# Performance work log

Measured on AMD Instinct MI355X. Metric: run time of the kernel, lower is better.

The kernel has to match this reference:

```python
import jax, jax.numpy as jnp
import numpy as np

S, N, E, D, HG, OG, L, B, HR = 8, 100000, 1600000, 64, 64, 64, 3, 128, 128
BN_EPS = 1e-5


def _glorot(k, shape):
    fan = shape[-2] + shape[-1]
    return jax.random.normal(k, shape, jnp.float32) * np.sqrt(2.0 / fan)


def setup_inputs() -> dict:
    key = jax.random.key(0)
    ks = jax.random.split(key, 16)
    xs = jax.random.normal(ks[0], (S, N, D), jnp.float32)
    edge_index = jax.random.randint(ks[1], (S, 2, E), 0, N, dtype=jnp.int32)
    batch = jnp.sort(jax.random.randint(ks[2], (N,), 0, B, dtype=jnp.int32))
    return {
        "xs": xs,
        "edge_index": edge_index,
        "batch": batch,
        # per-timestep, per-layer GIN MLP params (input_gnn == hidden_gnn == 64)
        "W1": _glorot(ks[3], (S, L, D, HG)),
        "b1": jnp.zeros((S, L, HG), jnp.float32),
        "gamma": jnp.ones((S, L, HG), jnp.float32),
        "beta": jnp.zeros((S, L, HG), jnp.float32),
        "W2": _glorot(ks[4], (S, L, HG, HG)),
        "b2": jnp.zeros((S, L, HG), jnp.float32),
        "Wg": _glorot(ks[5], (HG, OG)),
        "bg": jnp.zeros((OG,), jnp.float32),
        "Wih": _glorot(ks[6], (HR, OG)),
        "Whh": _glorot(ks[7], (HR, HR)),
        "bih": jnp.zeros((HR,), jnp.float32),
        "bhh": jnp.zeros((HR,), jnp.float32),
        "Wr": _glorot(ks[8], (1, HR)),
        "br": jnp.zeros((1,), jnp.float32),
        "batch_size": B,
    }


def _gnn_forward(xs, edge_index, batch, W1, b1, gamma, beta, W2, b2, Wg, bg,
                 Wih, Whh, bih, bhh, Wr, br, batch_size):
    n = xs.shape[1]
    pooled = []
    for t in range(S):  # small fixed seq_len; each timestep has distinct params
        x = xs[t]
        src, dst = edge_index[t, 0], edge_index[t, 1]
        for l in range(L):
            # GIN (eps=0): h_i = MLP(x_i + sum_{j->i} x_j)
            agg = jax.ops.segment_sum(x[src], dst, num_segments=n)
            h = x + agg
            h = h @ W1[t, l] + b1[t, l]
            # BatchNorm1d (training-mode stats over nodes, biased var)
            mu = jnp.mean(h, axis=0)
            var = jnp.var(h, axis=0)
            h = (h - mu) * jax.lax.rsqrt(var + BN_EPS) * gamma[t, l] + beta[t, l]
            h = jnp.tanh(h)
            h = jnp.tanh(h @ W2[t, l] + b2[t, l])
            x = h
        g = jax.ops.segment_sum(x, batch, num_segments=batch_size)  # global_add_pool
        pooled.append(g @ Wg + bg)
    h_seq = jnp.stack(pooled, axis=0)  # [S, B, OG]

    def rnn_step(hprev, xt):
        hnew = jnp.tanh(xt @ Wih.T + bih + hprev @ Whh.T + bhh)
        return hnew, None

    h0 = jnp.zeros((batch_size, HR), h_seq.dtype)
    h_last, _ = jax.lax.scan(rnn_step, h0, h_seq)
    return jax.nn.sigmoid(h_last @ Wr.T + br)  # [B, 1]


def reference(xs, edge_index, batch, W1, b1, gamma, beta, W2, b2, Wg, bg,
              Wih, Whh, bih, bhh, Wr, br, batch_size):
    return _gnn_forward(xs, edge_index, batch, W1, b1, gamma, beta, W2, b2,
                        Wg, bg, Wih, Whh, bih, bhh, Wr, br, batch_size)
```

## Files before the change

kernel.cpp:

```cpp
#include <hip/hip_runtime.h>
#include <math.h>

#define SQ 8
#define NN 100000
#define EE 1600000
#define LL 3
#define BB 128
#define HRR 128
#define ROWS 16
#define TILE 64
#define NTILE ((NN + TILE - 1) / TILE)
#define NBLK ((NN + 255) / 256)

__device__ __forceinline__ float fast_tanh(float x) {
    x = fminf(fmaxf(x, -15.f), 15.f);
    float e = __expf(2.f * x);
    return (e - 1.f) * __builtin_amdgcn_rcpf(e + 1.f);
}


__global__ void k_hist(const int* __restrict__ dst, int* __restrict__ deg) {
    int e = blockIdx.x * blockDim.x + threadIdx.x;
    if (e < EE) atomicAdd(&deg[dst[e]], 1);
}

__global__ void k_scan1(const int* __restrict__ deg, int* __restrict__ excl,
                        int* __restrict__ bsums) {
    __shared__ int buf[256];
    int tid = threadIdx.x;
    int i = blockIdx.x * 256 + tid;
    int v = (i < NN) ? deg[i] : 0;
    buf[tid] = v;
    __syncthreads();
    for (int off = 1; off < 256; off <<= 1) {
        int t = (tid >= off) ? buf[tid - off] : 0;
        __syncthreads();
        buf[tid] += t;
        __syncthreads();
    }
    if (i < NN) excl[i] = buf[tid] - v;
    if (tid == 255) bsums[blockIdx.x] = buf[255];
}

__global__ void k_scan2(const int* __restrict__ bsums, int* __restrict__ boff) {
    __shared__ int buf[512];
    int tid = threadIdx.x;
    int v = (tid < NBLK) ? bsums[tid] : 0;
    buf[tid] = v;
    __syncthreads();
    for (int off = 1; off < 512; off <<= 1) {
        int t = (tid >= off) ? buf[tid - off] : 0;
        __syncthreads();
        buf[tid] += t;
        __syncthreads();
    }
    if (tid < NBLK) boff[tid] = buf[tid] - v;
}

__global__ void k_scan3(int* __restrict__ row_start, const int* __restrict__ boff,
                        int* __restrict__ cursor) {
    int tid = threadIdx.x;
    int i = blockIdx.x * 256 + tid;
    if (i < NN) {
        int r = row_start[i] + boff[blockIdx.x];
        row_start[i] = r;
        cursor[i] = r;
    }
    if (blockIdx.x == 0 && tid == 0) row_start[NN] = EE;
}

__global__ void k_fill(const int* __restrict__ src, const int* __restrict__ dst,
                       int* __restrict__ cursor, int* __restrict__ csr) {
    int e = blockIdx.x * blockDim.x + threadIdx.x;
    if (e < EE) {
        int d = dst[e];
        int p = atomicAdd(&cursor[d], 1);
        csr[p] = src[e];
    }
}


__global__ __launch_bounds__(256, 6) void k_agg_mlp1(
    const float* __restrict__ xin, const int* __restrict__ row_start,
    const int* __restrict__ csr, const float* __restrict__ W1,
    const float* __restrict__ b1, float* __restrict__ h_out,
    float* __restrict__ stats) {
    __shared__ float sW[4096];
    __shared__ float sSum[4][64];
    __shared__ float sSq[4][64];
    int tid = threadIdx.x;
    for (int k = tid; k < 4096; k += 256) sW[k] = W1[k];
    __syncthreads();
    int wave = tid >> 6, lane = tid & 63;
    float bias = b1[lane];
    int base = blockIdx.x * TILE + wave * ROWS;
    float aS = 0.f, aQ = 0.f;
    for (int r = 0; r < ROWS; r++) {
        int i = base + r;
        if (i >= NN) break;
        float s = xin[(size_t)i * 64 + lane];
        int e0 = row_start[i], e1 = row_start[i + 1];
        int eb = e0;
        while (eb < e1) {
            int m = e1 - eb; if (m > 64) m = 64;
            int id = (lane < m) ? csr[eb + lane] : 0;
            int k = 0;
            for (; k + 8 <= m; k += 8) {
                const size_t o = lane;
                float v0 = xin[(size_t)__shfl(id, k + 0, 64) * 64 + o];
                float v1 = xin[(size_t)__shfl(id, k + 1, 64) * 64 + o];
                float v2 = xin[(size_t)__shfl(id, k + 2, 64) * 64 + o];
                float v3 = xin[(size_t)__shfl(id, k + 3, 64) * 64 + o];
                float v4 = xin[(size_t)__shfl(id, k + 4, 64) * 64 + o];
                float v5 = xin[(size_t)__shfl(id, k + 5, 64) * 64 + o];
                float v6 = xin[(size_t)__shfl(id, k + 6, 64) * 64 + o];
                float v7 = xin[(size_t)__shfl(id, k + 7, 64) * 64 + o];
                s += ((v0 + v1) + (v2 + v3)) + ((v4 + v5) + (v6 + v7));
            }
            for (; k + 2 <= m; k += 2) {
                float v0 = xin[(size_t)__shfl(id, k + 0, 64) * 64 + lane];
                float v1 = xin[(size_t)__shfl(id, k + 1, 64) * 64 + lane];
                s += v0 + v1;
            }
            for (; k < m; k++) s += xin[(size_t)__shfl(id, k, 64) * 64 + lane];
            eb += m;
        }
        float h0 = bias, h1 = 0.f, h2 = 0.f, h3 = 0.f;
#pragma unroll
        for (int c = 0; c < 64; c += 4) {
            h0 = fmaf(__shfl(s, c + 0, 64), sW[(c + 0) * 64 + lane], h0);
            h1 = fmaf(__shfl(s, c + 1, 64), sW[(c + 1) * 64 + lane], h1);
            h2 = fmaf(__shfl(s, c + 2, 64), sW[(c + 2) * 64 + lane], h2);
            h3 = fmaf(__shfl(s, c + 3, 64), sW[(c + 3) * 64 + lane], h3);
        }
        float h = (h0 + h1) + (h2 + h3);
        h_out[(size_t)i * 64 + lane] = h;
        aS += h;
        aQ += h * h;
    }
    sSum[wave][lane] = aS;
    sSq[wave][lane] = aQ;
    __syncthreads();
    if (wave == 0) {
        float s4 = sSum[0][lane] + sSum[1][lane] + sSum[2][lane] + sSum[3][lane];
        float q4 = sSq[0][lane] + sSq[1][lane] + sSq[2][lane] + sSq[3][lane];
        atomicAdd(&stats[lane], s4);
        atomicAdd(&stats[64 + lane], q4);
    }
}


__global__ __launch_bounds__(256, 6) void k_bn_mlp2(
    const float* __restrict__ h_in, const float* __restrict__ W2,
    const float* __restrict__ b2, const float* __restrict__ gamma,
    const float* __restrict__ beta, const float* __restrict__ stats,
    float* __restrict__ x_out, float* __restrict__ g_pool,
    const int* __restrict__ batch) {
    __shared__ float sW[4096];
    int tid = threadIdx.x;
    for (int k = tid; k < 4096; k += 256) sW[k] = W2[k];
    __syncthreads();
    int wave = tid >> 6, lane = tid & 63;
    float bias = b2[lane];
    float mu = stats[lane] * (1.0f / NN);
    float var = stats[64 + lane] * (1.0f / NN) - mu * mu;
    float scale = rsqrtf(var + 1e-5f) * gamma[lane];
    float shift = beta[lane] - mu * scale;
    int base = blockIdx.x * TILE + wave * ROWS;
    float pacc = 0.f;
    int pbid = -1;
    for (int r = 0; r < ROWS; r++) {
        int i = base + r;
        if (i >= NN) break;
        float v = h_in[(size_t)i * 64 + lane];
        float s = fast_tanh(fmaf(v, scale, shift));
        float h0 = bias, h1 = 0.f, h2 = 0.f, h3 = 0.f;
#pragma unroll
        for (int c = 0; c < 64; c += 4) {
            h0 = fmaf(__shfl(s, c + 0, 64), sW[(c + 0) * 64 + lane], h0);
            h1 = fmaf(__shfl(s, c + 1, 64), sW[(c + 1) * 64 + lane], h1);
            h2 = fmaf(__shfl(s, c + 2, 64), sW[(c + 2) * 64 + lane], h2);
            h3 = fmaf(__shfl(s, c + 3, 64), sW[(c + 3) * 64 + lane], h3);
        }
        float o = fast_tanh((h0 + h1) + (h2 + h3));
        if (x_out) {
            x_out[(size_t)i * 64 + lane] = o;
        } else {
            int bid = batch[i];
            if (bid != pbid) {
                if (pbid >= 0) atomicAdd(&g_pool[pbid * 64 + lane], pacc);
                pacc = 0.f;
                pbid = bid;
            }
            pacc += o;
        }
    }
    if (g_pool && pbid >= 0) atomicAdd(&g_pool[pbid * 64 + lane], pacc);
}


__global__ void k_pool_proj(const float* __restrict__ g_all, const float* __restrict__ Wg,
                            const float* __restrict__ bg, float* __restrict__ seq) {
    int idx = blockIdx.x * 256 + threadIdx.x;
    int o = idx & 63, row = idx >> 6;
    float acc = bg[o];
    const float* g = g_all + (size_t)row * 64;
#pragma unroll 8
    for (int c = 0; c < 64; c++) acc = fmaf(g[c], Wg[c * 64 + o], acc);
    seq[idx] = acc;
}

__global__ void k_transpose(const float* __restrict__ in, float* __restrict__ out,
                            int rows, int cols) {
    int idx = blockIdx.x * blockDim.x + threadIdx.x;
    if (idx < rows * cols) {
        int r = idx / cols, c = idx % cols;
        out[c * rows + r] = in[idx];
    }
}

__global__ __launch_bounds__(128) void k_rnn_all(
    const float* __restrict__ seq, const float* __restrict__ WihT,
    const float* __restrict__ WhhT, const float* __restrict__ bih,
    const float* __restrict__ bhh, const float* __restrict__ Wr,
    const float* __restrict__ br, float* __restrict__ out) {
    int b = blockIdx.x, j = threadIdx.x;
    __shared__ float sh[128];
    __shared__ float sx[64];
    __shared__ float sp[128];
    sh[j] = 0.f;
    float bsum = bih[j] + bhh[j];
    __syncthreads();
    for (int t = 0; t < SQ; t++) {
        if (j < 64) sx[j] = seq[((size_t)t * BB + b) * 64 + j];
        __syncthreads();
        float acc = bsum;
#pragma unroll 16
        for (int c = 0; c < 64; c++) acc = fmaf(sx[c], WihT[c * 128 + j], acc);
#pragma unroll 16
        for (int k = 0; k < 128; k++) acc = fmaf(sh[k], WhhT[k * 128 + j], acc);
        acc = tanhf(acc);
        __syncthreads();
        sh[j] = acc;
        __syncthreads();
    }
    sp[j] = sh[j] * Wr[j];
    __syncthreads();
    if (j == 0) {
        float a = br[0];
        for (int k = 0; k < 128; k++) a += sp[k];
        out[b] = 1.f / (1.f + expf(-a));
    }
}


extern "C" void kernel_launch(void* const* d_in, const int* in_sizes, int n_in,
                              void* d_out, int out_size, void* d_ws, size_t ws_size,
                              hipStream_t stream) {
    const float* xs    = (const float*)d_in[0];
    const int*   edge  = (const int*)d_in[1];
    const int*   batch = (const int*)d_in[2];
    const float* W1    = (const float*)d_in[3];
    const float* b1    = (const float*)d_in[4];
    const float* gamma = (const float*)d_in[5];
    const float* beta  = (const float*)d_in[6];
    const float* W2    = (const float*)d_in[7];
    const float* b2    = (const float*)d_in[8];
    const float* Wg    = (const float*)d_in[9];
    const float* bg    = (const float*)d_in[10];
    const float* Wih   = (const float*)d_in[11];
    const float* Whh   = (const float*)d_in[12];
    const float* bih   = (const float*)d_in[13];
    const float* bhh   = (const float*)d_in[14];
    const float* Wr    = (const float*)d_in[15];
    const float* br    = (const float*)d_in[16];

    char* p = (char*)d_ws;
    auto alloc = [&](size_t bytes) -> char* {
        char* r = p;
        p += (bytes + 255) & ~(size_t)255;
        return r;
    };
    float* x_cur     = (float*)alloc((size_t)NN * 64 * 4);
    float* h_tmp     = (float*)alloc((size_t)NN * 64 * 4);
    float* g_all     = (float*)alloc((size_t)SQ * BB * 64 * 4);
    float* seq       = (float*)alloc((size_t)SQ * BB * 64 * 4);
    float* WihT      = (float*)alloc((size_t)64 * HRR * 4);
    float* WhhT      = (float*)alloc((size_t)HRR * HRR * 4);
    float* stats     = (float*)alloc((size_t)SQ * LL * 128 * 4);
    int*   row_start = (int*)alloc((size_t)(NN + 1) * 4);
    int*   cursor    = (int*)alloc((size_t)NN * 4);
    int*   deg       = (int*)alloc((size_t)NN * 4);
    int*   csr       = (int*)alloc((size_t)EE * 4);
    int*   bsums     = (int*)alloc(512 * 4);
    int*   boff      = (int*)alloc(512 * 4);

    hipMemsetAsync(stats, 0, (size_t)SQ * LL * 128 * 4, stream);
    hipMemsetAsync(g_all, 0, (size_t)SQ * BB * 64 * 4, stream);
    k_transpose<<<(128 * 64 + 255) / 256, 256, 0, stream>>>(Wih, WihT, 128, 64);
    k_transpose<<<(128 * 128 + 255) / 256, 256, 0, stream>>>(Whh, WhhT, 128, 128);

    int ghist = EE / 256;
    for (int t = 0; t < SQ; t++) {
        const int* src = edge + (size_t)t * 2 * EE;
        const int* dst = src + EE;
        hipMemsetAsync(deg, 0, (size_t)NN * 4, stream);
        k_hist<<<ghist, 256, 0, stream>>>(dst, deg);
        k_scan1<<<NBLK, 256, 0, stream>>>(deg, row_start, bsums);
        k_scan2<<<1, 512, 0, stream>>>(bsums, boff);
        k_scan3<<<NBLK, 256, 0, stream>>>(row_start, boff, cursor);
        k_fill<<<ghist, 256, 0, stream>>>(src, dst, cursor, csr);
        for (int l = 0; l < LL; l++) {
            int pl = t * LL + l;
            const float* xin = (l == 0) ? xs + (size_t)t * NN * 64 : x_cur;
            k_agg_mlp1<<<NTILE, 256, 0, stream>>>(xin, row_start, csr,
                                                  W1 + (size_t)pl * 4096, b1 + (size_t)pl * 64,
                                                  h_tmp, stats + (size_t)pl * 128);
            k_bn_mlp2<<<NTILE, 256, 0, stream>>>(h_tmp, W2 + (size_t)pl * 4096,
                                                 b2 + (size_t)pl * 64, gamma + (size_t)pl * 64,
                                                 beta + (size_t)pl * 64, stats + (size_t)pl * 128,
                                                 (l < 2) ? x_cur : nullptr,
                                                 (l == 2) ? (g_all + (size_t)t * BB * 64) : nullptr,
                                                 batch);
        }
    }
    k_pool_proj<<<SQ * BB * 64 / 256, 256, 0, stream>>>(g_all, Wg, bg, seq);
    k_rnn_all<<<BB, 128, 0, stream>>>(seq, WihT, WhhT, bih, bhh, Wr, br, (float*)d_out);
}
```

Before: 7.727 ms.

## Process four nodes per wave with float4 gathers in aggregation+MLP1 kernel

Rewrites the aggregation/MLP1 kernel so each wave handles four nodes at once, with 16 lanes per node each loading a float4 (16 bytes) of the feature row instead of one float per lane. Neighbor ids are fetched 16 at a time per node, and the loop runs until every node in the wave is done. The 64x64 matvec becomes a per-lane float4 output computation, and the BN statistics are reduced with xor shuffles before the atomics. This aims to cut per-edge instruction and latency overhead in the gather, at the cost of divergence when nodes in a wave have different degrees, and wasted masked loads on padded slots.

```diff
diff --git a/kernel.cpp b/kernel.cpp
--- a/kernel.cpp
+++ b/kernel.cpp
@@ -7,7 +7,6 @@
 #define LL 3
 #define BB 128
 #define HRR 128
-#define ROWS 16
 #define TILE 64
 #define NTILE ((NN + TILE - 1) / TILE)
 #define NBLK ((NN + 255) / 256)
@@ -86,66 +85,98 @@
     const float* __restrict__ b1, float* __restrict__ h_out,
     float* __restrict__ stats) {
     __shared__ float sW[4096];
-    __shared__ float sSum[4][64];
-    __shared__ float sSq[4][64];
+    __shared__ float4 sS[4][16];
+    __shared__ float4 sQ[4][16];
     int tid = threadIdx.x;
     for (int k = tid; k < 4096; k += 256) sW[k] = W1[k];
     __syncthreads();
     int wave = tid >> 6, lane = tid & 63;
-    float bias = b1[lane];
-    int base = blockIdx.x * TILE + wave * ROWS;
-    float aS = 0.f, aQ = 0.f;
-    for (int r = 0; r < ROWS; r++) {
-        int i = base + r;
-        if (i >= NN) break;
-        float s = xin[(size_t)i * 64 + lane];
-        int e0 = row_start[i], e1 = row_start[i + 1];
-        int eb = e0;
-        while (eb < e1) {
-            int m = e1 - eb; if (m > 64) m = 64;
-            int id = (lane < m) ? csr[eb + lane] : 0;
-            int k = 0;
-            for (; k + 8 <= m; k += 8) {
-                const size_t o = lane;
-                float v0 = xin[(size_t)__shfl(id, k + 0, 64) * 64 + o];
-                float v1 = xin[(size_t)__shfl(id, k + 1, 64) * 64 + o];
-                float v2 = xin[(size_t)__shfl(id, k + 2, 64) * 64 + o];
-                float v3 = xin[(size_t)__shfl(id, k + 3, 64) * 64 + o];
-                float v4 = xin[(size_t)__shfl(id, k + 4, 64) * 64 + o];
-                float v5 = xin[(size_t)__shfl(id, k + 5, 64) * 64 + o];
-                float v6 = xin[(size_t)__shfl(id, k + 6, 64) * 64 + o];
-                float v7 = xin[(size_t)__shfl(id, k + 7, 64) * 64 + o];
-                s += ((v0 + v1) + (v2 + v3)) + ((v4 + v5) + (v6 + v7));
+    int sub = lane & 15;
+    int gbase = lane & 48;
+    float4 b4 = *(const float4*)&b1[sub * 4];
+    float4 aS = {0.f, 0.f, 0.f, 0.f}, aQ = {0.f, 0.f, 0.f, 0.f};
+    int nbase = blockIdx.x * TILE + wave * 16;
+    for (int r = 0; r < 4; r++) {
+        int i = nbase + r * 4 + (gbase >> 4);
+        bool valid = (i < NN);
+        int e0 = 0, e1 = 0;
+        float4 s0 = {0.f, 0.f, 0.f, 0.f}, s1 = {0.f, 0.f, 0.f, 0.f};
+        if (valid) {
+            e0 = row_start[i];
+            e1 = row_start[i + 1];
+            s0 = *(const float4*)&xin[(size_t)i * 64 + sub * 4];
+        }
+        for (int eb = e0; __any(eb < e1); eb += 16) {
+            int e = eb + sub;
+            int id = (e < e1) ? csr[e] : 0;
+#pragma unroll
+            for (int k = 0; k < 16; k += 2) {
+                int nb0 = __shfl(id, gbase + k, 64);
+                int nb1 = __shfl(id, gbase + k + 1, 64);
+                bool v0 = (eb + k) < e1;
+                bool v1 = (eb + k + 1) < e1;
+                float4 t0 = *(const float4*)&xin[(size_t)(v0 ? nb0 : 0) * 64 + sub * 4];
+                float4 t1 = *(const float4*)&xin[(size_t)(v1 ? nb1 : 0) * 64 + sub * 4];
+                if (v0) { s0.x += t0.x; s0.y += t0.y; s0.z += t0.z; s0.w += t0.w; }
+                if (v1) { s1.x += t1.x; s1.y += t1.y; s1.z += t1.z; s1.w += t1.w; }
             }
-            for (; k + 2 <= m; k += 2) {
-                float v0 = xin[(size_t)__shfl(id, k + 0, 64) * 64 + lane];
-                float v1 = xin[(size_t)__shfl(id, k + 1, 64) * 64 + lane];
-                s += v0 + v1;
-            }
-            for (; k < m; k++) s += xin[(size_t)__shfl(id, k, 64) * 64 + lane];
-            eb += m;
-        }
-        float h0 = bias, h1 = 0.f, h2 = 0.f, h3 = 0.f;
+        }
+        float4 s;
+        s.x = s0.x + s1.x; s.y = s0.y + s1.y; s.z = s0.z + s1.z; s.w = s0.w + s1.w;
+        float4 h0 = b4, h1 = {0.f, 0.f, 0.f, 0.f};
 #pragma unroll
         for (int c = 0; c < 64; c += 4) {
-            h0 = fmaf(__shfl(s, c + 0, 64), sW[(c + 0) * 64 + lane], h0);
-            h1 = fmaf(__shfl(s, c + 1, 64), sW[(c + 1) * 64 + lane], h1);
-            h2 = fmaf(__shfl(s, c + 2, 64), sW[(c + 2) * 64 + lane], h2);
-            h3 = fmaf(__shfl(s, c + 3, 64), sW[(c + 3) * 64 + lane], h3);
-        }
-        float h = (h0 + h1) + (h2 + h3);
-        h_out[(size_t)i * 64 + lane] = h;
-        aS += h;
-        aQ += h * h;
-    }
-    sSum[wave][lane] = aS;
-    sSq[wave][lane] = aQ;
-    __syncthreads();
-    if (wave == 0) {
-        float s4 = sSum[0][lane] + sSum[1][lane] + sSum[2][lane] + sSum[3][lane];
-        float q4 = sSq[0][lane] + sSq[1][lane] + sSq[2][lane] + sSq[3][lane];
-        atomicAdd(&stats[lane], s4);
-        atomicAdd(&stats[64 + lane], q4);
+            int srcl = gbase + (c >> 2);
+            float scx = __shfl(s.x, srcl, 64);
+            float scy = __shfl(s.y, srcl, 64);
+            float scz = __shfl(s.z, srcl, 64);
+            float scw = __shfl(s.w, srcl, 64);
+            float4 w0 = *(const float4*)&sW[(c + 0) * 64 + sub * 4];
+            float4 w1 = *(const float4*)&sW[(c + 1) * 64 + sub * 4];
+            float4 w2 = *(const float4*)&sW[(c + 2) * 64 + sub * 4];
+            float4 w3 = *(const float4*)&sW[(c + 3) * 64 + sub * 4];
+            h0.x = fmaf(scx, w0.x, h0.x); h0.y = fmaf(scx, w0.y, h0.y);
+            h0.z = fmaf(scx, w0.z, h0.z); h0.w = fmaf(scx, w0.w, h0.w);
+            h1.x = fmaf(scy, w1.x, h1.x); h1.y = fmaf(scy, w1.y, h1.y);
+            h1.z = fmaf(scy, w1.z, h1.z); h1.w = fmaf(scy, w1.w, h1.w);
+            h0.x = fmaf(scz, w2.x, h0.x); h0.y = fmaf(scz, w2.y, h0.y);
+            h0.z = fmaf(scz, w2.z, h0.z); h0.w = fmaf(scz, w2.w, h0.w);
+            h1.x = fmaf(scw, w3.x, h1.x); h1.y = fmaf(scw, w3.y, h1.y);
+            h1.z = fmaf(scw, w3.z, h1.z); h1.w = fmaf(scw, w3.w, h1.w);
+        }
+        float4 h;
+        h.x = h0.x + h1.x; h.y = h0.y + h1.y; h.z = h0.z + h1.z; h.w = h0.w + h1.w;
+        if (valid) {
+            *(float4*)&h_out[(size_t)i * 64 + sub * 4] = h;
+            aS.x += h.x; aS.y += h.y; aS.z += h.z; aS.w += h.w;
+            aQ.x += h.x * h.x; aQ.y += h.y * h.y; aQ.z += h.z * h.z; aQ.w += h.w * h.w;
+        }
+    }
+    aS.x += __shfl_xor(aS.x, 16, 64); aS.y += __shfl_xor(aS.y, 16, 64);
+    aS.z += __shfl_xor(aS.z, 16, 64); aS.w += __shfl_xor(aS.w, 16, 64);
+    aS.x += __shfl_xor(aS.x, 32, 64); aS.y += __shfl_xor(aS.y, 32, 64);
+    aS.z += __shfl_xor(aS.z, 32, 64); aS.w += __shfl_xor(aS.w, 32, 64);
+    aQ.x += __shfl_xor(aQ.x, 16, 64); aQ.y += __shfl_xor(aQ.y, 16, 64);
+    aQ.z += __shfl_xor(aQ.z, 16, 64); aQ.w += __shfl_xor(aQ.w, 16, 64);
+    aQ.x += __shfl_xor(aQ.x, 32, 64); aQ.y += __shfl_xor(aQ.y, 32, 64);
+    aQ.z += __shfl_xor(aQ.z, 32, 64); aQ.w += __shfl_xor(aQ.w, 32, 64);
+    if (lane < 16) { sS[wave][sub] = aS; sQ[wave][sub] = aQ; }
+    __syncthreads();
+    if (tid < 16) {
+        float4 s = sS[0][tid], q = sQ[0][tid];
+        for (int w = 1; w < 4; w++) {
+            float4 a = sS[w][tid], b = sQ[w][tid];
+            s.x += a.x; s.y += a.y; s.z += a.z; s.w += a.w;
+            q.x += b.x; q.y += b.y; q.z += b.z; q.w += b.w;
+        }
+        atomicAdd(&stats[tid * 4 + 0], s.x);
+        atomicAdd(&stats[tid * 4 + 1], s.y);
+        atomicAdd(&stats[tid * 4 + 2], s.z);
+        atomicAdd(&stats[tid * 4 + 3], s.w);
+        atomicAdd(&stats[64 + tid * 4 + 0], q.x);
+        atomicAdd(&stats[64 + tid * 4 + 1], q.y);
+        atomicAdd(&stats[64 + tid * 4 + 2], q.z);
+        atomicAdd(&stats[64 + tid * 4 + 3], q.w);
     }
 }
 
@@ -166,10 +197,10 @@
     float var = stats[64 + lane] * (1.0f / NN) - mu * mu;
     float scale = rsqrtf(var + 1e-5f) * gamma[lane];
     float shift = beta[lane] - mu * scale;
-    int base = blockIdx.x * TILE + wave * ROWS;
+    int base = blockIdx.x * TILE + wave * 16;
     float pacc = 0.f;
     int pbid = -1;
-    for (int r = 0; r < ROWS; r++) {
+    for (int r = 0; r < 16; r++) {
         int i = base + r;
         if (i >= NN) break;
         float v = h_in[(size_t)i * 64 + lane];
```

Result: slower. 13.21 ms (+71.0%).
